# Performance work log

Measured on AMD Instinct MI355X. Metric: run time of the kernel, lower is better.

Reference implementation:

```python
import jax, jax.numpy as jnp
import numpy as np

B, S, H, E = 16384, 128, 128, 64  # batch, state_dim, lstm hidden, context feature dim


def _lin(k, out_d, in_d, scale=0.05):
    kw, kb = jax.random.split(k)
    return (jax.random.normal(kw, (out_d, in_d), dtype=jnp.float32) * scale,
            jax.random.normal(kb, (out_d,), dtype=jnp.float32) * scale)


def setup_inputs() -> dict:
    key = jax.random.key(0)
    ks = jax.random.split(key, 24)
    d = {}
    d["goal_context"] = jax.random.normal(ks[0], (B, S), dtype=jnp.float32)
    d["sequence_length"] = 32
    # context encoder: 128 -> 256 -> 128 -> 64
    d["W1"], d["b1"] = _lin(ks[1], 256, S)
    d["W2"], d["b2"] = _lin(ks[2], 128, 256)
    d["W3"], d["b3"] = _lin(ks[3], E, 128)
    # 2-layer LSTM, hidden 128, input 128 (context zero-padded for step 0)
    d["Wih1"], d["bih1"] = _lin(ks[4], 4 * H, H)
    d["Whh1"], d["bhh1"] = _lin(ks[5], 4 * H, H)
    d["Wih2"], d["bih2"] = _lin(ks[6], 4 * H, H)
    d["Whh2"], d["bhh2"] = _lin(ks[7], 4 * H, H)
    # quality estimator: 192 -> 128 -> 64 -> 1
    d["Wq1"], d["bq1"] = _lin(ks[8], 128, H + E)
    d["Wq2"], d["bq2"] = _lin(ks[9], 64, 128)
    d["Wq3"], d["bq3"] = _lin(ks[10], 1, 64)
    # plan type head: 64 -> 32 -> 8
    d["Wp1"], d["bp1"] = _lin(ks[11], 32, E)
    d["Wp2"], d["bp2"] = _lin(ks[12], 8, 32)
    # duration predictor: 64 -> 32 -> 1
    d["Wd1"], d["bd1"] = _lin(ks[13], 32, E)
    d["Wd2"], d["bd2"] = _lin(ks[14], 1, 32)
    # cost predictor: 64 -> 32 -> 1
    d["Wc1"], d["bc1"] = _lin(ks[15], 32, E)
    d["Wc2"], d["bc2"] = _lin(ks[16], 1, 32)
    return d


def _lstm_cell(x, h, c, Wih, bih, Whh, bhh):
    g = x @ Wih.T + bih + h @ Whh.T + bhh
    i, f, gg, o = jnp.split(g, 4, axis=-1)
    c = jax.nn.sigmoid(f) * c + jax.nn.sigmoid(i) * jnp.tanh(gg)
    h = jax.nn.sigmoid(o) * jnp.tanh(c)
    return h, c


def reference(goal_context, sequence_length,
              W1, b1, W2, b2, W3, b3,
              Wih1, bih1, Whh1, bhh1, Wih2, bih2, Whh2, bhh2,
              Wq1, bq1, Wq2, bq2, Wq3, bq3,
              Wp1, bp1, Wp2, bp2,
              Wd1, bd1, Wd2, bd2,
              Wc1, bc1, Wc2, bc2):
    # context encoder (eval mode -> dropout is identity)
    h = jax.nn.relu(goal_context @ W1.T + b1)
    h = jax.nn.relu(h @ W2.T + b2)
    ctx = h @ W3.T + b3  # (B, 64)

    b = ctx.shape[0]
    x0 = jnp.pad(ctx, ((0, 0), (0, H - ctx.shape[-1])))  # (B, 128)
    z = jnp.zeros((b, H), dtype=ctx.dtype)

    def step(carry, _):
        x, h1, c1, h2, c2 = carry
        h1, c1 = _lstm_cell(x, h1, c1, Wih1, bih1, Whh1, bhh1)
        h2, c2 = _lstm_cell(h1, h2, c2, Wih2, bih2, Whh2, bhh2)
        return (h2, h1, c1, h2, c2), h2

    (x_final, _, _, _, _), seq = jax.lax.scan(step, (x0, z, z, z, z), None,
                                              length=sequence_length)
    action_sequence = jnp.transpose(seq, (1, 0, 2))  # (B, T, 128)

    q_in = jnp.concatenate([x_final, ctx], axis=-1)  # (B, 192)
    q = jax.nn.relu(q_in @ Wq1.T + bq1)
    q = jax.nn.relu(q @ Wq2.T + bq2)
    plan_quality = jax.nn.sigmoid(q @ Wq3.T + bq3)  # (B, 1)

    plan_type_probs = jax.nn.softmax(jax.nn.relu(ctx @ Wp1.T + bp1) @ Wp2.T + bp2, axis=-1)
    estimated_duration = jax.nn.relu(jax.nn.relu(ctx @ Wd1.T + bd1) @ Wd2.T + bd2)
    estimated_cost = jax.nn.relu(jax.nn.relu(ctx @ Wc1.T + bc1) @ Wc2.T + bc2)

    return (action_sequence, plan_quality, plan_type_probs,
            estimated_duration, estimated_cost, ctx)
```

## Files before the change

kernel.cpp:

```cpp
#include <hip/hip_runtime.h>
#include <cstdint>


typedef unsigned short u16;
typedef unsigned int   u32;
typedef float f32x4 __attribute__((ext_vector_type(4)));
typedef short s16x8 __attribute__((ext_vector_type(8)));
typedef int   i32x4 __attribute__((ext_vector_type(4)));

__device__ __forceinline__ u16 f2bf(float x) {
  u32 u = __float_as_uint(x);
  u32 r = u + 0x7fffu + ((u >> 16) & 1u);
  return (u16)(r >> 16);
}
__device__ __forceinline__ float bf2f(u16 v) { return __uint_as_float(((u32)v) << 16); }
__device__ __forceinline__ float fexp2(float x) { return __builtin_amdgcn_exp2f(x); }
__device__ __forceinline__ float frcp(float x)  { return __builtin_amdgcn_rcpf(x); }
__device__ __forceinline__ float sigf(float x)  { return frcp(1.f + fexp2(-1.4426950408889634f * x)); }

struct KParams {
  const float* gc;
  const float *W1, *b1, *W2, *b2, *W3, *b3;
  const float *Wih1, *bih1, *Whh1, *bhh1;
  const float *Wih2, *bih2, *Whh2, *bhh2;
  const float *Wq1, *bq1, *Wq2, *bq2, *Wq3, *bq3;
  const float *Wp1, *bp1, *Wp2, *bp2;
  const float *Wd1, *bd1, *Wd2, *bd2;
  const float *Wc1, *bc1, *Wc2, *bc2;
};

#define OW1   0
#define OW2   32768
#define OW3   65536
#define OWQ1  73728
#define OWQ2  106496
#define OWP1  114688
#define OWP2  116736
#define OWD1  117248
#define OWD2  119296
#define OWC1  119808
#define OWC2  121856
#define NBF16 122368
#define OWL1_B 245760
#define OWL2_B 376832
#define OFP32_B 507904

__global__ void prep_bf16(KParams P, u16* __restrict__ wsb, float* __restrict__ wsf) {
  int i = blockIdx.x * blockDim.x + threadIdx.x;
  int stride = gridDim.x * blockDim.x;
  for (; i < NBF16 + 1024; i += stride) {
    if (i < NBF16) {
      float v;
      int idx = i;
      if (idx < 32768) v = P.W1[idx];
      else if ((idx -= 32768) < 32768) v = P.W2[idx];
      else if ((idx -= 32768) < 8192)  v = P.W3[idx];
      else if ((idx -= 8192) < 32768) {
        int n = idx >> 8, k = idx & 255;
        v = (k < 192) ? P.Wq1[n * 192 + k] : 0.f;
      }
      else if ((idx -= 32768) < 8192) v = P.Wq2[idx];
      else if ((idx -= 8192) < 2048)  v = P.Wp1[idx];
      else if ((idx -= 2048) < 512) { int n = idx >> 5, k = idx & 31; v = (n < 8) ? P.Wp2[n * 32 + k] : 0.f; }
      else if ((idx -= 512) < 2048)  v = P.Wd1[idx];
      else if ((idx -= 2048) < 512) { int n = idx >> 5, k = idx & 31; v = (n < 1) ? P.Wd2[k] : 0.f; }
      else if ((idx -= 512) < 2048)  v = P.Wc1[idx];
      else { idx -= 2048; int n = idx >> 5, k = idx & 31; v = (n < 1) ? P.Wc2[k] : 0.f; }
      wsb[i] = f2bf(v);
    } else {
      int idx = i - NBF16;
      int l = idx >> 9, n = idx & 511;
      int gate = (n >> 4) & 3, j = ((n >> 6) << 4) | (n & 15);
      int orig = gate * 128 + j;
      wsf[idx] = (l == 0) ? (P.bih1[orig] + P.bhh1[orig]) : (P.bih2[orig] + P.bhh2[orig]);
    }
  }
}

__global__ void prep_lstm_q(KParams P, char* __restrict__ wsbytes, float* __restrict__ wsf) {
  int n = blockIdx.x;
  int lane = threadIdx.x;
  int l = n >> 9, nn = n & 511;
  int gate = (nn >> 4) & 3, j = ((nn >> 6) << 4) | (nn & 15);
  int orig = gate * 128 + j;
  float v[4];
#pragma unroll
  for (int i = 0; i < 4; ++i) {
    int k = lane * 4 + i;
    if (l == 0) v[i] = (k < 128) ? P.Wih1[orig * 128 + k] : P.Whh1[orig * 128 + (k - 128)];
    else        v[i] = (k < 128) ? P.Whh2[orig * 128 + k] : P.Wih2[orig * 128 + (k - 128)];
  }
  float m = fmaxf(fmaxf(fabsf(v[0]), fabsf(v[1])), fmaxf(fabsf(v[2]), fabsf(v[3])));
  for (int off = 1; off < 64; off <<= 1) m = fmaxf(m, __shfl_xor(m, off));
  float inv = (m > 1e-30f) ? 127.f / m : 0.f;
  u32 pk = 0;
#pragma unroll
  for (int i = 0; i < 4; ++i) {
    int q = (int)rintf(v[i] * inv);
    q = max(-127, min(127, q));
    pk |= ((u32)(q & 255)) << (8 * i);
  }
  *(u32*)(wsbytes + (l ? OWL2_B : OWL1_B) + nn * 256 + lane * 4) = pk;
  if (lane == 0) wsf[1024 + l * 512 + nn] = (m > 1e-30f) ? (m * (1.f / (127.f * 127.f))) : 0.f;
}

__device__ __forceinline__ void lds_wr_bf16(char* sD, int stride, int mask, int m, int n, float v) {
  int slot = ((n >> 3) + m) & mask;
  *(u16*)(sD + m * stride + (slot << 4) + (n & 7) * 2) = f2bf(v);
}

template <int K, int STRIDE, int MASK, int NT, class EPI>
__device__ __forceinline__ void gemm_generic(const char* sA, const u16* W,
                                             int w, int l16, int grp, EPI epi) {
  constexpr int KT = K / 32;
  constexpr int ITMAX = (NT + 7) / 8;
#pragma unroll
  for (int it = 0; it < ITMAX; ++it) {
    int tile = w + it * 8;
    if (tile < NT) {
      int mt = tile & 3, nt = tile >> 2;
      int row = mt * 16 + l16;
      const u16* wl = W + (size_t)(nt * 16 + l16) * K + grp * 8;
      f32x4 acc = (f32x4){0.f, 0.f, 0.f, 0.f};
#pragma unroll
      for (int kt = 0; kt < KT; ++kt) {
        int slot = (kt * 4 + grp + row) & MASK;
        s16x8 a = *(const s16x8*)(sA + row * STRIDE + (slot << 4));
        s16x8 b = *(const s16x8*)(wl + kt * 32);
        acc = __builtin_amdgcn_mfma_f32_16x16x32_bf16(a, b, acc, 0, 0, 0);
      }
      epi(it, mt, nt, acc);
    }
  }
}

__device__ __forceinline__ void ldb4q(const char* const (&wb)[4], int kt, i32x4 (&bd)[4]) {
#pragma unroll
  for (int g = 0; g < 4; ++g) bd[g] = *(const i32x4*)(wb[g] + kt * 64);
}

template <int KT0, int KT1>
__device__ __forceinline__ void lstm_gemm_i8(const char* X, const char* Hh,
                                             const int (&ha)[4][2],
                                             const char* const (&wb)[4],
                                             const i32x4 (&bpre)[4],
                                             i32x4 (&acc)[4][4]) {
  const i32x4 zc = (i32x4){0, 0, 0, 0};
  i32x4 bc[4], bn[4], ac[4], an[4];
#pragma unroll
  for (int g = 0; g < 4; ++g) bc[g] = bpre[g];
  {
    const char* base = (KT0 < 2) ? X : Hh;
#pragma unroll
    for (int mt = 0; mt < 4; ++mt) ac[mt] = *(const i32x4*)(base + ha[mt][KT0 & 1]);
  }
#pragma unroll
  for (int kt = KT0; kt < KT1; ++kt) {
    if (kt + 1 < KT1) {
      ldb4q(wb, kt + 1, bn);
      const char* base = (kt + 1 < 2) ? X : Hh;
#pragma unroll
      for (int mt = 0; mt < 4; ++mt) an[mt] = *(const i32x4*)(base + ha[mt][(kt + 1) & 1]);
    }
#pragma unroll
    for (int mt = 0; mt < 4; ++mt)
#pragma unroll
      for (int g = 0; g < 4; ++g)
        acc[mt][g] = __builtin_amdgcn_mfma_i32_16x16x64_i8(
            ac[mt], bc[g], (kt == KT0) ? zc : acc[mt][g], 0, 0, 0);
    if (kt + 1 < KT1) {
#pragma unroll
      for (int g = 0; g < 4; ++g) bc[g] = bn[g];
#pragma unroll
      for (int mt = 0; mt < 4; ++mt) ac[mt] = an[mt];
    }
  }
}

template <int KT0, int KT1>
__device__ __forceinline__ void lstm_gemm_l1(const char* X, const char* Hh,
                                             const int (&ha)[4][2],
                                             const char* wl1,
                                             const int (&wa)[4][4],
                                             i32x4 (&acc)[4][4]) {
  const i32x4 zc = (i32x4){0, 0, 0, 0};
#pragma unroll
  for (int kt = KT0; kt < KT1; ++kt) {
    const char* base = (kt < 2) ? X : Hh;
    i32x4 a[4], b[4];
#pragma unroll
    for (int g = 0; g < 4; ++g) b[g] = *(const i32x4*)(wl1 + wa[g][kt]);
#pragma unroll
    for (int mt = 0; mt < 4; ++mt) a[mt] = *(const i32x4*)(base + ha[mt][kt & 1]);
#pragma unroll
    for (int mt = 0; mt < 4; ++mt)
#pragma unroll
      for (int g = 0; g < 4; ++g)
        acc[mt][g] = __builtin_amdgcn_mfma_i32_16x16x64_i8(
            a[mt], b[g], (kt == KT0) ? zc : acc[mt][g], 0, 0, 0);
  }
}

template <int LAYER, bool FINAL>
__device__ __forceinline__ void lstm_update_i8(const i32x4 (&acc)[4][4], float (&cst)[4][4],
                                               const float (&bl)[4], const float (&dq)[4],
                                               float dqmul, char* dst, char* qbuf,
                                               int w, int l16, int grp,
                                               float* __restrict__ out0, int b0, int t) {
  const int j = w * 16 + l16;
  const float K1 = 1.4426950408889634f;
  const float K2 = 2.8853900817779268f;
  float kdq[4], kbl[4];
  kdq[0] = -K1 * dq[0] * dqmul; kbl[0] = -K1 * bl[0];
  kdq[1] = -K1 * dq[1] * dqmul; kbl[1] = -K1 * bl[1];
  kdq[2] = -K2 * dq[2] * dqmul; kbl[2] = -K2 * bl[2];
  kdq[3] = -K1 * dq[3] * dqmul; kbl[3] = -K1 * bl[3];
#pragma unroll
  for (int mt = 0; mt < 4; ++mt) {
#pragma unroll
    for (int r = 0; r < 4; ++r) {
      const int m = mt * 16 + grp * 4 + r;
      float ei = fexp2(fmaf((float)acc[mt][0][r], kdq[0], kbl[0]));
      float ef = fexp2(fmaf((float)acc[mt][1][r], kdq[1], kbl[1]));
      float eg = fexp2(fmaf((float)acc[mt][2][r], kdq[2], kbl[2]));
      float eo = fexp2(fmaf((float)acc[mt][3][r], kdq[3], kbl[3]));
      float D1 = 1.f + ef;
      float D2 = fmaf(ei, eg, 1.f + ei + eg);
      float num = fmaf(cst[mt][r], D2, (1.f - eg) * D1);
      float c = num * frcp(D1 * D2);
      cst[mt][r] = c;
      float ec = fexp2(c * -K2);
      float h = (1.f - ec) * frcp((1.f + eo) * (1.f + ec));
      if (!FINAL) {
        int q = (int)rintf(h * 127.f);
        *(char*)(dst + m * 128 + ((((j >> 4) + m) & 7) << 4) + (j & 15)) = (char)q;
      } else {
        *(u16*)(qbuf + m * 256 + ((((j >> 3) + m) & 15) << 4) + (j & 7) * 2) = f2bf(h);
      }
      if (LAYER == 1)
        out0[(size_t)(b0 + m) * 4096 + (size_t)t * 128 + j] = h;
    }
  }
}

__global__ __launch_bounds__(512, 2) void planning_fused(KParams P,
                                                         const u16* __restrict__ wsb,
                                                         const char* __restrict__ wsbytes,
                                                         const float* __restrict__ wsf,
                                                         float* __restrict__ out) {
  __shared__ __align__(16) char smem[163840];
  char* bufB = smem;
  char* bufA = smem + 16384;
  char* htmp = smem + 49152;
  char* CTXB = smem + 61440;
  char* WL1  = smem;
  char* X0   = smem + 131072;
  char* X1   = smem + 139264;
  char* H10  = smem + 147456;
  char* H11  = smem + 155648;
  char* QBUF = smem;
  char* CTX2 = smem + 16384;
  char* QL1  = smem + 32768;
  char* QL2  = smem + 49152;

  const int tid = threadIdx.x;
  const int lane = tid & 63;
  const int w = tid >> 6;
  const int l16 = lane & 15;
  const int grp = lane >> 4;
  const int b0 = blockIdx.x * 64;

  float* out0 = out;
  float* out1 = out + 67108864;
  float* out2 = out + 67125248;
  float* out3 = out + 67256320;
  float* out4 = out + 67272704;
  float* out5 = out + 67289088;

#pragma unroll
  for (int ii = 0; ii < 4; ++ii) {
    int idx = tid + ii * 512;
    int row = idx >> 5, c4 = idx & 31;
    f32x4 v = *(const f32x4*)(P.gc + (size_t)(b0 + row) * 128 + c4 * 4);
    u32 lo = (u32)f2bf(v[0]) | ((u32)f2bf(v[1]) << 16);
    u32 hi = (u32)f2bf(v[2]) | ((u32)f2bf(v[3]) << 16);
    int byte = row * 256 + ((((c4 >> 1) + row) & 15) << 4) + (c4 & 1) * 8;
    uint2 pk; pk.x = lo; pk.y = hi;
    *(uint2*)(bufB + byte) = pk;
  }
  __syncthreads();

  gemm_generic<128, 256, 15, 64>(bufB, wsb + OW1, w, l16, grp,
    [&](int, int mt, int nt, f32x4 a) {
      int n = nt * 16 + l16;
      float bias = P.b1[n];
#pragma unroll
      for (int r = 0; r < 4; ++r)
        lds_wr_bf16(bufA, 512, 31, mt * 16 + grp * 4 + r, n, fmaxf(a[r] + bias, 0.f));
    });
  __syncthreads();

  gemm_generic<256, 512, 31, 32>(bufA, wsb + OW2, w, l16, grp,
    [&](int, int mt, int nt, f32x4 a) {
      int n = nt * 16 + l16;
      float bias = P.b2[n];
#pragma unroll
      for (int r = 0; r < 4; ++r)
        lds_wr_bf16(bufB, 256, 15, mt * 16 + grp * 4 + r, n, fmaxf(a[r] + bias, 0.f));
    });
  __syncthreads();

  *(f32x4*)(X0 + tid * 16) = (f32x4){0.f, 0.f, 0.f, 0.f};
  f32x4 ctx3[2];
  gemm_generic<128, 256, 15, 16>(bufB, wsb + OW3, w, l16, grp,
    [&](int it, int, int, f32x4 a) { if (it == 0) ctx3[0] = a; else ctx3[1] = a; });
  __syncthreads();

#pragma unroll
  for (int it = 0; it < 2; ++it) {
    int tile = w + it * 8;
    int mt = tile & 3, nt = tile >> 2;
    int n = nt * 16 + l16;
    float bias = P.b3[n];
#pragma unroll
    for (int r = 0; r < 4; ++r) {
      int m = mt * 16 + grp * 4 + r;
      float v = ctx3[it][r] + bias;
      ctx3[it][r] = v;
      out5[(size_t)(b0 + m) * 64 + n] = v;
      *(u16*)(CTXB + m * 128 + ((((n >> 3) + m) & 7) << 4) + (n & 7) * 2) = f2bf(v);
      int q = (int)rintf(v * 63.5f);
      q = max(-127, min(127, q));
      *(char*)(X0 + m * 128 + ((((n >> 4) + m) & 7) << 4) + (n & 15)) = (char)q;
    }
  }
  __syncthreads();

#pragma unroll
  for (int hh = 0; hh < 3; ++hh) {
    const u16* Wh = (hh == 0) ? (wsb + OWP1) : (hh == 1) ? (wsb + OWD1) : (wsb + OWC1);
    const float* bh = (hh == 0) ? P.bp1 : (hh == 1) ? P.bd1 : P.bc1;
    char* dsth = htmp + hh * 4096;
    gemm_generic<64, 128, 7, 8>(CTXB, Wh, w, l16, grp,
      [&](int, int mt, int nt, f32x4 a) {
        int n = nt * 16 + l16;
        float bias = bh[n];
#pragma unroll
        for (int r = 0; r < 4; ++r)
          lds_wr_bf16(dsth, 64, 3, mt * 16 + grp * 4 + r, n, fmaxf(a[r] + bias, 0.f));
      });
  }
  __syncthreads();

#pragma unroll
  for (int it = 0; it < 2; ++it) {
    int tile = w + it * 8;
    if (tile < 12) {
      int head = tile >> 2, mt = tile & 3;
      int row = mt * 16 + l16;
      const char* aB = htmp + head * 4096;
      int slot = (grp + row) & 3;
      s16x8 a = *(const s16x8*)(aB + row * 64 + (slot << 4));
      const u16* W2h = (head == 0) ? (wsb + OWP2) : (head == 1) ? (wsb + OWD2) : (wsb + OWC2);
      s16x8 b = *(const s16x8*)(W2h + l16 * 32 + grp * 8);
      f32x4 acc = (f32x4){0.f, 0.f, 0.f, 0.f};
      acc = __builtin_amdgcn_mfma_f32_16x16x32_bf16(a, b, acc, 0, 0, 0);
      if (head == 0) {
        float bp = (l16 < 8) ? P.bp2[l16] : 0.f;
#pragma unroll
        for (int r = 0; r < 4; ++r) {
          int m = mt * 16 + grp * 4 + r;
          float v = (l16 < 8) ? (acc[r] + bp) : -3.0e38f;
          float mx = v;
          mx = fmaxf(mx, __shfl_xor(mx, 1));
          mx = fmaxf(mx, __shfl_xor(mx, 2));
          mx = fmaxf(mx, __shfl_xor(mx, 4));
          mx = fmaxf(mx, __shfl_xor(mx, 8));
          float e = (l16 < 8) ? fexp2(1.4426950408889634f * (v - mx)) : 0.f;
          float s = e;
          s += __shfl_xor(s, 1); s += __shfl_xor(s, 2);
          s += __shfl_xor(s, 4); s += __shfl_xor(s, 8);
          if (l16 < 8) out2[(size_t)(b0 + m) * 8 + l16] = e * frcp(s);
        }
      } else {
        float bb = (head == 1) ? P.bd2[0] : P.bc2[0];
        float* dst = (head == 1) ? out3 : out4;
        if (l16 == 0) {
#pragma unroll
          for (int r = 0; r < 4; ++r) {
            int m = mt * 16 + grp * 4 + r;
            dst[b0 + m] = fmaxf(acc[r] + bb, 0.f);
          }
        }
      }
    }
  }
  __syncthreads();

#pragma unroll
  for (int it = 0; it < 16; ++it) {
    int c = tid + it * 512;
    int n = c >> 4, s = c & 15;
    f32x4 v = *(const f32x4*)(wsbytes + OWL1_B + (size_t)c * 16);
    *(f32x4*)(WL1 + n * 256 + ((s ^ (n & 15)) << 4)) = v;
  }
  __syncthreads();

  int ha[4][2];
#pragma unroll
  for (int mt = 0; mt < 4; ++mt) {
    int row = mt * 16 + l16;
#pragma unroll
    for (int k2 = 0; k2 < 2; ++k2)
      ha[mt][k2] = row * 128 + (((k2 * 4 + grp + row) & 7) << 4);
  }
  int wa[4][4];
#pragma unroll
  for (int g = 0; g < 4; ++g) {
    int n = w * 64 + g * 16 + l16;
#pragma unroll
    for (int kt = 0; kt < 4; ++kt)
      wa[g][kt] = n * 256 + (((kt * 4 + grp) ^ l16) << 4);
  }
  const char* wb2[4];
  float bl1[4], bl2[4], dq1[4], dq2[4];
#pragma unroll
  for (int g = 0; g < 4; ++g) {
    int nn = w * 64 + g * 16 + l16;
    wb2[g] = wsbytes + OWL2_B + (size_t)nn * 256 + grp * 16;
    bl1[g] = wsf[nn];          bl2[g] = wsf[512 + nn];
    dq1[g] = wsf[1024 + nn];   dq2[g] = wsf[1536 + nn];
  }
  float cst1[4][4], cst2[4][4];
#pragma unroll
  for (int a = 0; a < 4; ++a)
#pragma unroll
    for (int b = 0; b < 4; ++b) { cst1[a][b] = 0.f; cst2[a][b] = 0.f; }

  {
    i32x4 acc[4][4];
    lstm_gemm_l1<0, 2>(X0, H10, ha, WL1, wa, acc);
    i32x4 bq[4]; ldb4q(wb2, 2, bq);
    lstm_update_i8<0, false>(acc, cst1, bl1, dq1, 2.f, H11, QBUF, w, l16, grp, out0, b0, 0);
    __syncthreads();
    lstm_gemm_i8<2, 4>(X0, H11, ha, wb2, bq, acc);
    lstm_update_i8<1, false>(acc, cst2, bl2, dq2, 1.f, X1, QBUF, w, l16, grp, out0, b0, 0);
    __syncthreads();
  }
  for (int t = 1; t < 31; ++t) {
    const char* Xr = (t & 1) ? X1 : X0;
    char*       Xw = (t & 1) ? X0 : X1;
    const char* Hr = (t & 1) ? H11 : H10;
    char*       Hw = (t & 1) ? H10 : H11;
    i32x4 acc[4][4];
    lstm_gemm_l1<0, 4>(Xr, Hr, ha, WL1, wa, acc);
    i32x4 bq[4]; ldb4q(wb2, 0, bq);
    lstm_update_i8<0, false>(acc, cst1, bl1, dq1, 1.f, Hw, QBUF, w, l16, grp, out0, b0, t);
    __syncthreads();
    lstm_gemm_i8<0, 4>(Xr, Hw, ha, wb2, bq, acc);
    lstm_update_i8<1, false>(acc, cst2, bl2, dq2, 1.f, Xw, QBUF, w, l16, grp, out0, b0, t);
    __syncthreads();
  }
  {
    i32x4 acc[4][4];
    lstm_gemm_l1<0, 4>(X1, H11, ha, WL1, wa, acc);
    i32x4 bq[4]; ldb4q(wb2, 0, bq);
    lstm_update_i8<0, false>(acc, cst1, bl1, dq1, 1.f, H10, QBUF, w, l16, grp, out0, b0, 31);
    __syncthreads();
    lstm_gemm_i8<0, 4>(X1, H10, ha, wb2, bq, acc);
    lstm_update_i8<1, true>(acc, cst2, bl2, dq2, 1.f, X0, QBUF, w, l16, grp, out0, b0, 31);
    __syncthreads();
  }

#pragma unroll
  for (int it = 0; it < 2; ++it) {
    int tile = w + it * 8;
    int mt = tile & 3, nt = tile >> 2;
    int n = nt * 16 + l16;
#pragma unroll
    for (int r = 0; r < 4; ++r) {
      int m = mt * 16 + grp * 4 + r;
      *(u16*)(CTX2 + m * 128 + ((((n >> 3) + m) & 7) << 4) + (n & 7) * 2) = f2bf(ctx3[it][r]);
    }
  }
  __syncthreads();

  int hb[4][4];
#pragma unroll
  for (int mt = 0; mt < 4; ++mt) {
    int row = mt * 16 + l16;
#pragma unroll
    for (int k4 = 0; k4 < 4; ++k4)
      hb[mt][k4] = row * 256 + (((k4 * 4 + grp + row) & 15) << 4);
  }
#pragma unroll
  for (int it = 0; it < 4; ++it) {
    int tile = w + it * 8;
    int mt = tile & 3, nt = tile >> 2;
    int row = mt * 16 + l16;
    const u16* wl = wsb + OWQ1 + (size_t)(nt * 16 + l16) * 256 + grp * 8;
    f32x4 acc = (f32x4){0.f, 0.f, 0.f, 0.f};
#pragma unroll
    for (int kt = 0; kt < 4; ++kt) {
      s16x8 a = *(const s16x8*)(QBUF + hb[mt][kt]);
      s16x8 b = *(const s16x8*)(wl + kt * 32);
      acc = __builtin_amdgcn_mfma_f32_16x16x32_bf16(a, b, acc, 0, 0, 0);
    }
#pragma unroll
    for (int kc = 0; kc < 2; ++kc) {
      s16x8 a = *(const s16x8*)(CTX2 + row * 128 + (((kc * 4 + grp + row) & 7) << 4));
      s16x8 b = *(const s16x8*)(wl + (4 + kc) * 32);
      acc = __builtin_amdgcn_mfma_f32_16x16x32_bf16(a, b, acc, 0, 0, 0);
    }
    int n = nt * 16 + l16;
    float bias = P.bq1[n];
#pragma unroll
    for (int r = 0; r < 4; ++r)
      lds_wr_bf16(QL1, 256, 15, mt * 16 + grp * 4 + r, n, fmaxf(acc[r] + bias, 0.f));
  }
  __syncthreads();

  gemm_generic<128, 256, 15, 16>(QL1, wsb + OWQ2, w, l16, grp,
    [&](int, int mt, int nt, f32x4 a) {
      int n = nt * 16 + l16;
      float bias = P.bq2[n];
#pragma unroll
      for (int r = 0; r < 4; ++r)
        lds_wr_bf16(QL2, 128, 7, mt * 16 + grp * 4 + r, n, fmaxf(a[r] + bias, 0.f));
    });
  __syncthreads();

  {
    int m = tid >> 3, k8 = (tid & 7) * 8;
    int slot = ((k8 >> 3) + m) & 7;
    s16x8 qv = *(const s16x8*)(QL2 + m * 128 + (slot << 4));
    float s = 0.f;
#pragma unroll
    for (int i = 0; i < 8; ++i) s += bf2f((u16)qv[i]) * P.Wq3[k8 + i];
    s += __shfl_xor(s, 1); s += __shfl_xor(s, 2); s += __shfl_xor(s, 4);
    if ((lane & 7) == 0) out1[b0 + m] = sigf(s + P.bq3[0]);
  }
}

extern "C" void kernel_launch(void* const* d_in, const int* in_sizes, int n_in,
                              void* d_out, int out_size, void* d_ws, size_t ws_size,
                              hipStream_t stream) {
  (void)in_sizes; (void)n_in; (void)out_size; (void)ws_size;
  KParams P;
  P.gc   = (const float*)d_in[0];
  P.W1   = (const float*)d_in[2];  P.b1   = (const float*)d_in[3];
  P.W2   = (const float*)d_in[4];  P.b2   = (const float*)d_in[5];
  P.W3   = (const float*)d_in[6];  P.b3   = (const float*)d_in[7];
  P.Wih1 = (const float*)d_in[8];  P.bih1 = (const float*)d_in[9];
  P.Whh1 = (const float*)d_in[10]; P.bhh1 = (const float*)d_in[11];
  P.Wih2 = (const float*)d_in[12]; P.bih2 = (const float*)d_in[13];
  P.Whh2 = (const float*)d_in[14]; P.bhh2 = (const float*)d_in[15];
  P.Wq1  = (const float*)d_in[16]; P.bq1  = (const float*)d_in[17];
  P.Wq2  = (const float*)d_in[18]; P.bq2  = (const float*)d_in[19];
  P.Wq3  = (const float*)d_in[20]; P.bq3  = (const float*)d_in[21];
  P.Wp1  = (const float*)d_in[22]; P.bp1  = (const float*)d_in[23];
  P.Wp2  = (const float*)d_in[24]; P.bp2  = (const float*)d_in[25];
  P.Wd1  = (const float*)d_in[26]; P.bd1  = (const float*)d_in[27];
  P.Wd2  = (const float*)d_in[28]; P.bd2  = (const float*)d_in[29];
  P.Wc1  = (const float*)d_in[30]; P.bc1  = (const float*)d_in[31];
  P.Wc2  = (const float*)d_in[32]; P.bc2  = (const float*)d_in[33];

  u16*   wsb     = (u16*)d_ws;
  char*  wsbytes = (char*)d_ws;
  float* wsf     = (float*)((char*)d_ws + OFP32_B);

  prep_bf16<<<483, 256, 0, stream>>>(P, wsb, wsf);
  prep_lstm_q<<<1024, 64, 0, stream>>>(P, wsbytes, wsf);
  planning_fused<<<256, 512, 0, stream>>>(P, wsb, wsbytes, wsf, (float*)d_out);
}
```

Baseline: 338.8 us.

## Hoist layer-2 input GEMM before layer-1 update and precompute gate scale constants

Splits the layer-2 LSTM GEMM into an input part (X, known before layer 1 finishes) and a recurrent part (new h1). The X part now runs right after the layer-1 GEMM, before the layer-1 elementwise update and barrier, so less work waits on the critical path after the sync. Gate scale and bias constants are precomputed once outside the time loop, and the output stores are made nontemporal. The cost is higher register pressure from holding two accumulator sets (acc1, acc2) plus weight fragments, which may spill under launch_bounds(512,2).

```diff
diff --git a/kernel.cpp b/kernel.cpp
--- a/kernel.cpp
+++ b/kernel.cpp
@@ -139,42 +139,48 @@
   for (int g = 0; g < 4; ++g) bd[g] = *(const i32x4*)(wb[g] + kt * 64);
 }
 
-template <int KT0, int KT1>
-__device__ __forceinline__ void lstm_gemm_i8(const char* X, const char* Hh,
-                                             const int (&ha)[4][2],
-                                             const char* const (&wb)[4],
-                                             const i32x4 (&bpre)[4],
+__device__ __forceinline__ void lstm_gemm2_X(const char* X, const int (&ha)[4][2],
+                                             const i32x4 (&bx0)[4], const i32x4 (&bx1)[4],
                                              i32x4 (&acc)[4][4]) {
   const i32x4 zc = (i32x4){0, 0, 0, 0};
-  i32x4 bc[4], bn[4], ac[4], an[4];
-#pragma unroll
-  for (int g = 0; g < 4; ++g) bc[g] = bpre[g];
-  {
-    const char* base = (KT0 < 2) ? X : Hh;
-#pragma unroll
-    for (int mt = 0; mt < 4; ++mt) ac[mt] = *(const i32x4*)(base + ha[mt][KT0 & 1]);
-  }
-#pragma unroll
-  for (int kt = KT0; kt < KT1; ++kt) {
-    if (kt + 1 < KT1) {
-      ldb4q(wb, kt + 1, bn);
-      const char* base = (kt + 1 < 2) ? X : Hh;
-#pragma unroll
-      for (int mt = 0; mt < 4; ++mt) an[mt] = *(const i32x4*)(base + ha[mt][(kt + 1) & 1]);
-    }
-#pragma unroll
-    for (int mt = 0; mt < 4; ++mt)
-#pragma unroll
-      for (int g = 0; g < 4; ++g)
-        acc[mt][g] = __builtin_amdgcn_mfma_i32_16x16x64_i8(
-            ac[mt], bc[g], (kt == KT0) ? zc : acc[mt][g], 0, 0, 0);
-    if (kt + 1 < KT1) {
-#pragma unroll
-      for (int g = 0; g < 4; ++g) bc[g] = bn[g];
-#pragma unroll
-      for (int mt = 0; mt < 4; ++mt) ac[mt] = an[mt];
-    }
-  }
+  i32x4 a0[4], a1[4];
+#pragma unroll
+  for (int mt = 0; mt < 4; ++mt) a0[mt] = *(const i32x4*)(X + ha[mt][0]);
+#pragma unroll
+  for (int mt = 0; mt < 4; ++mt) a1[mt] = *(const i32x4*)(X + ha[mt][1]);
+#pragma unroll
+  for (int mt = 0; mt < 4; ++mt)
+#pragma unroll
+    for (int g = 0; g < 4; ++g)
+      acc[mt][g] = __builtin_amdgcn_mfma_i32_16x16x64_i8(a0[mt], bx0[g], zc, 0, 0, 0);
+#pragma unroll
+  for (int mt = 0; mt < 4; ++mt)
+#pragma unroll
+    for (int g = 0; g < 4; ++g)
+      acc[mt][g] = __builtin_amdgcn_mfma_i32_16x16x64_i8(a1[mt], bx1[g], acc[mt][g], 0, 0, 0);
+}
+
+template <bool ZSTART>
+__device__ __forceinline__ void lstm_gemm2_H(const char* Hh, const int (&ha)[4][2],
+                                             const i32x4 (&bh2)[4], const i32x4 (&bh3)[4],
+                                             i32x4 (&acc)[4][4]) {
+  const i32x4 zc = (i32x4){0, 0, 0, 0};
+  i32x4 a0[4], a1[4];
+#pragma unroll
+  for (int mt = 0; mt < 4; ++mt) a0[mt] = *(const i32x4*)(Hh + ha[mt][0]);
+#pragma unroll
+  for (int mt = 0; mt < 4; ++mt) a1[mt] = *(const i32x4*)(Hh + ha[mt][1]);
+#pragma unroll
+  for (int mt = 0; mt < 4; ++mt)
+#pragma unroll
+    for (int g = 0; g < 4; ++g)
+      acc[mt][g] = __builtin_amdgcn_mfma_i32_16x16x64_i8(
+          a0[mt], bh2[g], ZSTART ? zc : acc[mt][g], 0, 0, 0);
+#pragma unroll
+  for (int mt = 0; mt < 4; ++mt)
+#pragma unroll
+    for (int g = 0; g < 4; ++g)
+      acc[mt][g] = __builtin_amdgcn_mfma_i32_16x16x64_i8(a1[mt], bh3[g], acc[mt][g], 0, 0, 0);
 }
 
 template <int KT0, int KT1>
@@ -203,18 +209,12 @@
 
 template <int LAYER, bool FINAL>
 __device__ __forceinline__ void lstm_update_i8(const i32x4 (&acc)[4][4], float (&cst)[4][4],
-                                               const float (&bl)[4], const float (&dq)[4],
-                                               float dqmul, char* dst, char* qbuf,
+                                               const float (&kdq)[4], const float (&kbl)[4],
+                                               char* dst, char* qbuf,
                                                int w, int l16, int grp,
                                                float* __restrict__ out0, int b0, int t) {
   const int j = w * 16 + l16;
-  const float K1 = 1.4426950408889634f;
   const float K2 = 2.8853900817779268f;
-  float kdq[4], kbl[4];
-  kdq[0] = -K1 * dq[0] * dqmul; kbl[0] = -K1 * bl[0];
-  kdq[1] = -K1 * dq[1] * dqmul; kbl[1] = -K1 * bl[1];
-  kdq[2] = -K2 * dq[2] * dqmul; kbl[2] = -K2 * bl[2];
-  kdq[3] = -K1 * dq[3] * dqmul; kbl[3] = -K1 * bl[3];
 #pragma unroll
   for (int mt = 0; mt < 4; ++mt) {
 #pragma unroll
@@ -238,7 +238,7 @@
         *(u16*)(qbuf + m * 256 + ((((j >> 3) + m) & 15) << 4) + (j & 7) * 2) = f2bf(h);
       }
       if (LAYER == 1)
-        out0[(size_t)(b0 + m) * 4096 + (size_t)t * 128 + j] = h;
+        __builtin_nontemporal_store(h, &out0[(size_t)(b0 + m) * 4096 + (size_t)t * 128 + j]);
     }
   }
 }
@@ -423,13 +423,19 @@
       wa[g][kt] = n * 256 + (((kt * 4 + grp) ^ l16) << 4);
   }
   const char* wb2[4];
-  float bl1[4], bl2[4], dq1[4], dq2[4];
-#pragma unroll
-  for (int g = 0; g < 4; ++g) {
-    int nn = w * 64 + g * 16 + l16;
-    wb2[g] = wsbytes + OWL2_B + (size_t)nn * 256 + grp * 16;
-    bl1[g] = wsf[nn];          bl2[g] = wsf[512 + nn];
-    dq1[g] = wsf[1024 + nn];   dq2[g] = wsf[1536 + nn];
+  float kdq1[4], kbl1[4], kdq2[4], kbl2[4], kdq1a[4];
+  {
+    const float K1 = 1.4426950408889634f, K2 = 2.8853900817779268f;
+#pragma unroll
+    for (int g = 0; g < 4; ++g) {
+      int nn = w * 64 + g * 16 + l16;
+      wb2[g] = wsbytes + OWL2_B + (size_t)nn * 256 + grp * 16;
+      float bl1v = wsf[nn], bl2v = wsf[512 + nn];
+      float dq1v = wsf[1024 + nn], dq2v = wsf[1536 + nn];
+      float kk = (g == 2) ? K2 : K1;
+      kdq1[g] = -kk * dq1v;  kdq1a[g] = -kk * dq1v * 2.f;  kbl1[g] = -kk * bl1v;
+      kdq2[g] = -kk * dq2v;  kbl2[g] = -kk * bl2v;
+    }
   }
   float cst1[4][4], cst2[4][4];
 #pragma unroll
@@ -438,13 +444,14 @@
     for (int b = 0; b < 4; ++b) { cst1[a][b] = 0.f; cst2[a][b] = 0.f; }
 
   {
-    i32x4 acc[4][4];
-    lstm_gemm_l1<0, 2>(X0, H10, ha, WL1, wa, acc);
-    i32x4 bq[4]; ldb4q(wb2, 2, bq);
-    lstm_update_i8<0, false>(acc, cst1, bl1, dq1, 2.f, H11, QBUF, w, l16, grp, out0, b0, 0);
+    i32x4 acc1[4][4], acc2[4][4];
+    lstm_gemm_l1<0, 2>(X0, H10, ha, WL1, wa, acc1);
+    i32x4 bh2[4], bh3[4];
+    ldb4q(wb2, 2, bh2); ldb4q(wb2, 3, bh3);
+    lstm_update_i8<0, false>(acc1, cst1, kdq1a, kbl1, H11, QBUF, w, l16, grp, out0, b0, 0);
     __syncthreads();
-    lstm_gemm_i8<2, 4>(X0, H11, ha, wb2, bq, acc);
-    lstm_update_i8<1, false>(acc, cst2, bl2, dq2, 1.f, X1, QBUF, w, l16, grp, out0, b0, 0);
+    lstm_gemm2_H<true>(H11, ha, bh2, bh3, acc2);
+    lstm_update_i8<1, false>(acc2, cst2, kdq2, kbl2, X1, QBUF, w, l16, grp, out0, b0, 0);
     __syncthreads();
   }
   for (int t = 1; t < 31; ++t) {
@@ -452,23 +459,31 @@
     char*       Xw = (t & 1) ? X0 : X1;
     const char* Hr = (t & 1) ? H11 : H10;
     char*       Hw = (t & 1) ? H10 : H11;
-    i32x4 acc[4][4];
-    lstm_gemm_l1<0, 4>(Xr, Hr, ha, WL1, wa, acc);
-    i32x4 bq[4]; ldb4q(wb2, 0, bq);
-    lstm_update_i8<0, false>(acc, cst1, bl1, dq1, 1.f, Hw, QBUF, w, l16, grp, out0, b0, t);
+    i32x4 acc1[4][4], acc2[4][4];
+    lstm_gemm_l1<0, 4>(Xr, Hr, ha, WL1, wa, acc1);
+    i32x4 bx0[4], bx1[4];
+    ldb4q(wb2, 0, bx0); ldb4q(wb2, 1, bx1);
+    lstm_gemm2_X(Xr, ha, bx0, bx1, acc2);
+    i32x4 bh2[4], bh3[4];
+    ldb4q(wb2, 2, bh2); ldb4q(wb2, 3, bh3);
+    lstm_update_i8<0, false>(acc1, cst1, kdq1, kbl1, Hw, QBUF, w, l16, grp, out0, b0, t);
     __syncthreads();
-    lstm_gemm_i8<0, 4>(Xr, Hw, ha, wb2, bq, acc);
-    lstm_update_i8<1, false>(acc, cst2, bl2, dq2, 1.f, Xw, QBUF, w, l16, grp, out0, b0, t);
+    lstm_gemm2_H<false>(Hw, ha, bh2, bh3, acc2);
+    lstm_update_i8<1, false>(acc2, cst2, kdq2, kbl2, Xw, QBUF, w, l16, grp, out0, b0, t);
     __syncthreads();
   }
   {
-    i32x4 acc[4][4];
-    lstm_gemm_l1<0, 4>(X1, H11, ha, WL1, wa, acc);
-    i32x4 bq[4]; ldb4q(wb2, 0, bq);
-    lstm_update_i8<0, false>(acc, cst1, bl1, dq1, 1.f, H10, QBUF, w, l16, grp, out0, b0, 31);
+    i32x4 acc1[4][4], acc2[4][4];
+    lstm_gemm_l1<0, 4>(X1, H11, ha, WL1, wa, acc1);
+    i32x4 bx0[4], bx1[4];
+    ldb4q(wb2, 0, bx0); ldb4q(wb2, 1, bx1);
+    lstm_gemm2_X(X1, ha, bx0, bx1, acc2);
+    i32x4 bh2[4], bh3[4];
+    ldb4q(wb2, 2, bh2); ldb4q(wb2, 3, bh3);
+    lstm_update_i8<0, false>(acc1, cst1, kdq1, kbl1, H10, QBUF, w, l16, grp, out0, b0, 31);
     __syncthreads();
-    lstm_gemm_i8<0, 4>(X1, H10, ha, wb2, bq, acc);
-    lstm_update_i8<1, true>(acc, cst2, bl2, dq2, 1.f, X0, QBUF, w, l16, grp, out0, b0, 31);
+    lstm_gemm2_H<false>(H10, ha, bh2, bh3, acc2);
+    lstm_update_i8<1, true>(acc2, cst2, kdq2, kbl2, X0, QBUF, w, l16, grp, out0, b0, 31);
     __syncthreads();
   }
 
```

Result: slower. 397.0 us (+17.2%).
